# Optimization experiments

Measured on AMD Instinct MI355X. Metric: run time of the kernel, lower is better.

The kernel has to match this reference:

```python
import jax, jax.numpy as jnp
import numpy as np
from jax import lax

CH = 128
COND_CH = 80
N_LAYERS = 4
KSIZE = 3
KC = CH * CH * KSIZE * N_LAYERS  # 196608 kernel channels
BC = CH * N_LAYERS               # 512 bias channels


def _conv1d(x, w, b, padding, dilation=1):
    # x: [B, Cin, T], w: [Cout, Cin, K], b: [Cout]
    y = lax.conv_general_dilated(
        x, w, window_strides=(1,), padding=[(padding, padding)],
        rhs_dilation=(dilation,), dimension_numbers=("NCW", "OIW", "NCW"))
    return y + b[None, :, None]


def setup_inputs() -> dict:
    key = jax.random.key(0)
    ks = jax.random.split(key, 10)
    B, T_audio, T_mel = 8, 16384, 32
    scale = 0.02
    return {
        "x": jax.random.normal(ks[0], (B, CH, T_audio), jnp.float32),
        "cond": jax.random.normal(ks[1], (B, COND_CH, T_mel), jnp.float32),
        # predictor net params
        "w0": jax.random.normal(ks[2], (64, COND_CH, 5), jnp.float32) * scale,
        "b0": jnp.zeros((64,), jnp.float32),
        "w1": jax.random.normal(ks[3], (64, 64, 3), jnp.float32) * scale,
        "b1": jnp.zeros((64,), jnp.float32),
        "w2": jax.random.normal(ks[4], (KC + BC, 64, 1), jnp.float32) * scale,
        "b2": jnp.zeros((KC + BC,), jnp.float32),
        # snake activation param
        "alpha": jnp.ones((1, CH, 1), jnp.float32),
    }


def reference(x, cond, w0, b0, w1, b1, w2, b2, alpha):
    # --- kernel predictor ---
    h = jax.nn.gelu(_conv1d(cond, w0, b0, padding=2), approximate=False)
    h = jax.nn.gelu(_conv1d(h, w1, b1, padding=1), approximate=False)
    out = _conv1d(h, w2, b2, padding=0)          # [B, KC+BC, T_mel]
    kernels_flat = out[:, :KC]                    # [B, KC, T_mel]
    biases_flat = out[:, KC:]                     # [B, BC, T_mel]

    B = x.shape[0]
    k_per_layer = CH * CH * KSIZE

    def per_sample_conv(xi, ki, dilation, pad):
        # xi: [ch, T], ki: [ch, ch, ksize]
        y = lax.conv_general_dilated(
            xi[None], ki, window_strides=(1,), padding=[(pad, pad)],
            rhs_dilation=(dilation,), dimension_numbers=("NCW", "OIW", "NCW"))
        return y[0]

    for i in range(N_LAYERS):
        k_flat = kernels_flat[:, i * k_per_layer:(i + 1) * k_per_layer]
        b_flat = biases_flat[:, i * CH:(i + 1) * CH]
        dilation = 2 ** i
        pad = dilation * (KSIZE - 1) // 2
        k_mean = k_flat.mean(axis=-1).reshape(B, CH, CH, KSIZE)
        b_mean = b_flat.mean(axis=-1)             # [B, ch]
        y = jax.vmap(per_sample_conv, in_axes=(0, 0, None, None))(x, k_mean, dilation, pad)
        x = y + b_mean[:, :, None] + x            # conv(+bias) with residual

    # snake activation: x + 1/(alpha+eps) * sin(alpha*x)^2
    return x + 1.0 / (alpha + 1e-08) * jnp.sin(alpha * x) ** 2
```

## Files before the change

kernel.cpp:

```cpp
#include <hip/hip_runtime.h>
#include <math.h>

#define CHN 128
#define TT 16384
#define NBATCH 8
#define KCONST 196608
#define TILE_T 64
#define GUARD 8
#define CRANGE 96
#define ROWS 112
#define LROW 136

typedef __bf16 bf16x8 __attribute__((ext_vector_type(8)));
typedef float  f32x4  __attribute__((ext_vector_type(4)));
typedef unsigned short u16x8 __attribute__((ext_vector_type(8)));
typedef unsigned short u16x4 __attribute__((ext_vector_type(4)));

__device__ __forceinline__ unsigned short f2bf(float f) {
    union { float f; unsigned int u; } v; v.f = f;
    unsigned int u = v.u;
    u += 0x7fffu + ((u >> 16) & 1u);
    return (unsigned short)(u >> 16);
}
__device__ __forceinline__ float b2f(unsigned short h) {
    union { float f; unsigned int u; } v; v.u = ((unsigned int)h) << 16;
    return v.f;
}

__device__ __forceinline__ float gelu_exact(float x) {
    return 0.5f * x * (1.0f + erff(x * 0.70710678118654752f));
}

__global__ __launch_bounds__(256) void k_cond0(
    const float* __restrict__ cond, const float* __restrict__ w0,
    const float* __restrict__ b0, float* __restrict__ h0)
{
    __shared__ float cS[80 * 32];
    __shared__ float wS[8 * 80 * 5];
    __shared__ float bS[8];
    int b = blockIdx.x >> 3, g = blockIdx.x & 7;
    int tid = threadIdx.x;

    for (int idx = tid; idx < 80 * 32; idx += 256) cS[idx] = cond[b * 2560 + idx];
    for (int idx = tid; idx < 8 * 400; idx += 256) wS[idx] = w0[g * 3200 + idx];
    if (tid < 8) bS[tid] = b0[g * 8 + tid];
    __syncthreads();

    int oc = tid >> 5, t = tid & 31;
    float acc = bS[oc];
    const float* wr = wS + oc * 400;
    for (int ic = 0; ic < 80; ++ic) {
        const float* cr = cS + ic * 32;
        #pragma unroll
        for (int j = 0; j < 5; ++j) {
            int tv = t - 2 + j;
            if (tv >= 0 && tv < 32) acc += wr[ic * 5 + j] * cr[tv];
        }
    }
    h0[(b * 64 + g * 8 + oc) * 32 + t] = gelu_exact(acc);
}

__global__ __launch_bounds__(256) void k_cond1(
    const float* __restrict__ h0, const float* __restrict__ w1,
    const float* __restrict__ b1, float* __restrict__ hbar)
{
    __shared__ float hS[64 * 32];
    __shared__ float wS[8 * 64 * 3];
    __shared__ float bS[8];
    int b = blockIdx.x >> 3, g = blockIdx.x & 7;
    int tid = threadIdx.x;

    for (int idx = tid; idx < 64 * 32; idx += 256) hS[idx] = h0[b * 2048 + idx];
    for (int idx = tid; idx < 8 * 192; idx += 256) wS[idx] = w1[g * 1536 + idx];
    if (tid < 8) bS[tid] = b1[g * 8 + tid];
    __syncthreads();

    int oc = tid >> 5, t = tid & 31;
    float acc = bS[oc];
    const float* wr = wS + oc * 192;
    for (int ic = 0; ic < 64; ++ic) {
        const float* hr = hS + ic * 32;
        #pragma unroll
        for (int j = 0; j < 3; ++j) {
            int tv = t - 1 + j;
            if (tv >= 0 && tv < 32) acc += wr[ic * 3 + j] * hr[tv];
        }
    }
    float v = gelu_exact(acc);
    #pragma unroll
    for (int off = 1; off < 32; off <<= 1) v += __shfl_xor(v, off, 64);
    if (t == 0) hbar[b * 64 + g * 8 + oc] = v * (1.0f / 32.0f);
}

__global__ __launch_bounds__(256) void k_weights(
    const float* __restrict__ w2, const float* __restrict__ b2,
    const float* __restrict__ hbar,
    unsigned short* __restrict__ W, float* __restrict__ bmean)
{
    __shared__ float hS[8 * 64];
    __shared__ float buf[256 * 68];
    int tid = threadIdx.x;
    for (int idx = tid; idx < 512; idx += 256) hS[idx] = hbar[idx];

    const float4* src4 = (const float4*)(w2 + (long)blockIdx.x * 16384);
    #pragma unroll
    for (int it = 0; it < 16; ++it) {
        int f = it * 256 + tid;
        float4 v = src4[f];
        int row = f >> 4, col = f & 15;
        *(float4*)&buf[row * 68 + col * 4] = v;
    }
    __syncthreads();

    long p = (long)blockIdx.x * 256 + tid;
    const float* rowp = &buf[tid * 68];
    float acc[8];
    #pragma unroll
    for (int bb = 0; bb < 8; ++bb) acc[bb] = 0.f;
    #pragma unroll
    for (int q = 0; q < 16; ++q) {
        float4 wv = *(const float4*)&rowp[q * 4];
        #pragma unroll
        for (int bb = 0; bb < 8; ++bb) {
            const float* h = hS + bb * 64 + q * 4;
            acc[bb] += wv.x * h[0] + wv.y * h[1] + wv.z * h[2] + wv.w * h[3];
        }
    }
    float bias = b2[p];
    if (p < KCONST) {
        int i = (int)(p / 49152); int r = (int)(p % 49152);
        int o = r / 384; int m = r % 384; int c = m / 3; int tp = m % 3;
        #pragma unroll
        for (int bb = 0; bb < 8; ++bb)
            W[(long)((bb * 4 + i) * 128 + o) * 384 + tp * 128 + c] =
                f2bf(acc[bb] + bias);
    } else {
        int q = (int)(p - KCONST); int i = q >> 7, o = q & 127;
        #pragma unroll
        for (int bb = 0; bb < 8; ++bb)
            bmean[(bb * 4 + i) * 128 + o] = acc[bb] + bias;
    }
}

__global__ __launch_bounds__(256, 2) void k_fused(
    const float* __restrict__ src, float* __restrict__ dst,
    const unsigned short* __restrict__ W, const float* __restrict__ bmean,
    const float* __restrict__ alpha)
{
    __shared__ __align__(16) unsigned short xhi[ROWS * LROW];
    __shared__ __align__(16) unsigned short xlo[ROWS * LROW];

    int tid  = threadIdx.x;
    int lane = tid & 63;
    int wave = tid >> 6;
    int b    = blockIdx.x >> 8;
    int tile = blockIdx.x & 255;
    int T0   = tile * TILE_T;

    int nrow = lane & 15;
    int quad = lane >> 4;
    int o0   = wave * 32;

    const float* xb = src + (long)b * CHN * TT;

    {
        int cb = wave * 32;
        #pragma unroll 1
        for (int pass = 0; pass < 2; ++pass) {
            int tl = pass * 64 + lane;
            if (tl < ROWS) {
                int tg = T0 - 24 + tl;
                bool ok = (tg >= 0) && (tg < TT);
                #pragma unroll
                for (int kb = 0; kb < 4; ++kb) {
                    float v[8];
                    #pragma unroll
                    for (int k = 0; k < 8; ++k)
                        v[k] = ok ? xb[(long)(cb + kb * 8 + k) * TT + tg] : 0.f;
                    u16x8 h, l;
                    #pragma unroll
                    for (int k = 0; k < 8; ++k) {
                        h[k] = f2bf(v[k]);
                        l[k] = f2bf(v[k] - b2f(h[k]));
                    }
                    *(u16x8*)&xhi[tl * LROW + cb + kb * 8] = h;
                    *(u16x8*)&xlo[tl * LROW + cb + kb * 8] = l;
                }
            }
        }
    }

    float aval[2][4];
    #pragma unroll
    for (int mt = 0; mt < 2; ++mt)
        #pragma unroll
        for (int r = 0; r < 4; ++r)
            aval[mt][r] = alpha[o0 + mt * 16 + quad * 4 + r];

    __syncthreads();

    #pragma unroll 1
    for (int l = 0; l < 4; ++l) {
        const int d = 1 << l;
        const unsigned short* Wl = W + (long)((b * 4 + l) * 128) * 384;
        const float* bm = bmean + (b * 4 + l) * 128;

        bf16x8 af[2][12];
        #pragma unroll
        for (int mt = 0; mt < 2; ++mt) {
            const unsigned short* wr =
                Wl + (long)(o0 + mt * 16 + nrow) * 384 + quad * 8;
            #pragma unroll
            for (int ks = 0; ks < 12; ++ks)
                af[mt][ks] = *(const bf16x8*)(wr + ks * 32);
        }
        float bias[2][4];
        #pragma unroll
        for (int mt = 0; mt < 2; ++mt)
            #pragma unroll
            for (int r = 0; r < 4; ++r)
                bias[mt][r] = bm[o0 + mt * 16 + quad * 4 + r];

        f32x4 acc[2][6];
        #pragma unroll
        for (int mt = 0; mt < 2; ++mt)
            #pragma unroll
            for (int nt = 0; nt < 6; ++nt)
                acc[mt][nt] = (f32x4){0.f, 0.f, 0.f, 0.f};

        #pragma unroll
        for (int ks = 0; ks < 12; ++ks) {
            const int c0 = (ks & 3) * 32 + quad * 8;
            const int roff = GUARD + nrow + ((ks >> 2) - 1) * d;
            #pragma unroll
            for (int nt = 0; nt < 6; ++nt) {
                bf16x8 bf = *(const bf16x8*)&xhi[(roff + nt * 16) * LROW + c0];
                acc[0][nt] = __builtin_amdgcn_mfma_f32_16x16x32_bf16(
                    af[0][ks], bf, acc[0][nt], 0, 0, 0);
                acc[1][nt] = __builtin_amdgcn_mfma_f32_16x16x32_bf16(
                    af[1][ks], bf, acc[1][nt], 0, 0, 0);
            }
        }

        #pragma unroll
        for (int mt = 0; mt < 2; ++mt) {
            int obase = o0 + mt * 16 + quad * 4;
            #pragma unroll
            for (int nt = 0; nt < 6; ++nt) {
                int trow = GUARD + nt * 16 + nrow;
                u16x4 rh = *(const u16x4*)&xhi[trow * LROW + obase];
                u16x4 rl = *(const u16x4*)&xlo[trow * LROW + obase];
                #pragma unroll
                for (int r = 0; r < 4; ++r)
                    acc[mt][nt][r] += b2f(rh[r]) + b2f(rl[r]) + bias[mt][r];
            }
        }
        __syncthreads();

        if (l < 3) {
            #pragma unroll
            for (int mt = 0; mt < 2; ++mt) {
                int obase = o0 + mt * 16 + quad * 4;
                #pragma unroll
                for (int nt = 0; nt < 6; ++nt) {
                    int trow = GUARD + nt * 16 + nrow;
                    int tg = T0 - 16 + nt * 16 + nrow;
                    bool ok = ((unsigned)tg < (unsigned)TT);
                    u16x4 h, lo4;
                    #pragma unroll
                    for (int r = 0; r < 4; ++r) {
                        float v = ok ? acc[mt][nt][r] : 0.f;
                        h[r]   = f2bf(v);
                        lo4[r] = f2bf(v - b2f(h[r]));
                    }
                    *(u16x4*)&xhi[trow * LROW + obase] = h;
                    *(u16x4*)&xlo[trow * LROW + obase] = lo4;
                }
            }
            __syncthreads();
        } else {
            #pragma unroll
            for (int mt = 0; mt < 2; ++mt) {
                #pragma unroll
                for (int r = 0; r < 4; ++r) {
                    int o = o0 + mt * 16 + quad * 4 + r;
                    float av = aval[mt][r];
                    long rowoff = ((long)b * CHN + o) * TT + T0;
                    #pragma unroll
                    for (int nt = 1; nt < 5; ++nt) {
                        int t = (nt - 1) * 16 + nrow;
                        float xn = acc[mt][nt][r];
                        float s = sinf(av * xn);
                        dst[rowoff + t] = xn + (1.0f / (av + 1e-8f)) * s * s;
                    }
                }
            }
        }
    }
}

extern "C" void kernel_launch(void* const* d_in, const int* in_sizes, int n_in,
                              void* d_out, int out_size, void* d_ws, size_t ws_size,
                              hipStream_t stream) {
    const float* x     = (const float*)d_in[0];
    const float* cond  = (const float*)d_in[1];
    const float* w0    = (const float*)d_in[2];
    const float* b0    = (const float*)d_in[3];
    const float* w1    = (const float*)d_in[4];
    const float* b1    = (const float*)d_in[5];
    const float* w2    = (const float*)d_in[6];
    const float* b2    = (const float*)d_in[7];
    const float* alpha = (const float*)d_in[8];
    float* out = (float*)d_out;

    char* ws = (char*)d_ws;
    unsigned short* W = (unsigned short*)ws;
    float* bmean = (float*)(ws + 3145728);
    float* hbar  = (float*)(ws + 3162112);
    float* h0    = (float*)(ws + 3164160);

    k_cond0<<<64, 256, 0, stream>>>(cond, w0, b0, h0);
    k_cond1<<<64, 256, 0, stream>>>(h0, w1, b1, hbar);
    k_weights<<<772, 256, 0, stream>>>(w2, b2, hbar, W, bmean);
    k_fused<<<2048, 256, 0, stream>>>(x, out, W, bmean, alpha);
}
```

Measured before the change: 363.9 us.

## Carry residual in fp32 accumulators, drop lo LDS buffer, raise occupancy

Removes the second (low-bits) shared-memory activation buffer. The residual is now kept in fp32 accumulators that persist across layers, and layer 0 reads the input residual straight from global memory. This halves LDS use and stops preloading all weight fragments into registers, which allows launch_bounds of 4 blocks per CU. Weight fragments are loaded from global memory per k-step, and the final snake activation uses __sinf with a hoisted reciprocal, trading some accuracy for speed.

```diff
diff --git a/kernel.cpp b/kernel.cpp
--- a/kernel.cpp
+++ b/kernel.cpp
@@ -142,13 +142,12 @@
     }
 }
 
-__global__ __launch_bounds__(256, 2) void k_fused(
+__global__ __launch_bounds__(256, 4) void k_fused(
     const float* __restrict__ src, float* __restrict__ dst,
     const unsigned short* __restrict__ W, const float* __restrict__ bmean,
     const float* __restrict__ alpha)
 {
     __shared__ __align__(16) unsigned short xhi[ROWS * LROW];
-    __shared__ __align__(16) unsigned short xlo[ROWS * LROW];
 
     int tid  = threadIdx.x;
     int lane = tid & 63;
@@ -177,25 +176,21 @@
                     #pragma unroll
                     for (int k = 0; k < 8; ++k)
                         v[k] = ok ? xb[(long)(cb + kb * 8 + k) * TT + tg] : 0.f;
-                    u16x8 h, l;
-                    #pragma unroll
-                    for (int k = 0; k < 8; ++k) {
-                        h[k] = f2bf(v[k]);
-                        l[k] = f2bf(v[k] - b2f(h[k]));
-                    }
+                    u16x8 h;
+                    #pragma unroll
+                    for (int k = 0; k < 8; ++k) h[k] = f2bf(v[k]);
                     *(u16x8*)&xhi[tl * LROW + cb + kb * 8] = h;
-                    *(u16x8*)&xlo[tl * LROW + cb + kb * 8] = l;
-                }
-            }
-        }
-    }
-
-    float aval[2][4];
+                }
+            }
+        }
+    }
+
+    f32x4 acc[2][6];
     #pragma unroll
     for (int mt = 0; mt < 2; ++mt)
         #pragma unroll
-        for (int r = 0; r < 4; ++r)
-            aval[mt][r] = alpha[o0 + mt * 16 + quad * 4 + r];
+        for (int nt = 0; nt < 6; ++nt)
+            acc[mt][nt] = (f32x4){0.f, 0.f, 0.f, 0.f};
 
     __syncthreads();
 
@@ -205,54 +200,55 @@
         const unsigned short* Wl = W + (long)((b * 4 + l) * 128) * 384;
         const float* bm = bmean + (b * 4 + l) * 128;
 
-        bf16x8 af[2][12];
-        #pragma unroll
-        for (int mt = 0; mt < 2; ++mt) {
-            const unsigned short* wr =
-                Wl + (long)(o0 + mt * 16 + nrow) * 384 + quad * 8;
-            #pragma unroll
-            for (int ks = 0; ks < 12; ++ks)
-                af[mt][ks] = *(const bf16x8*)(wr + ks * 32);
-        }
-        float bias[2][4];
-        #pragma unroll
-        for (int mt = 0; mt < 2; ++mt)
-            #pragma unroll
-            for (int r = 0; r < 4; ++r)
-                bias[mt][r] = bm[o0 + mt * 16 + quad * 4 + r];
-
-        f32x4 acc[2][6];
-        #pragma unroll
-        for (int mt = 0; mt < 2; ++mt)
-            #pragma unroll
-            for (int nt = 0; nt < 6; ++nt)
-                acc[mt][nt] = (f32x4){0.f, 0.f, 0.f, 0.f};
-
         #pragma unroll
         for (int ks = 0; ks < 12; ++ks) {
             const int c0 = (ks & 3) * 32 + quad * 8;
             const int roff = GUARD + nrow + ((ks >> 2) - 1) * d;
+            const unsigned short* wr =
+                Wl + (long)(o0 + nrow) * 384 + ks * 32 + quad * 8;
+            bf16x8 a0 = *(const bf16x8*)(wr);
+            bf16x8 a1 = *(const bf16x8*)(wr + 16 * 384);
             #pragma unroll
             for (int nt = 0; nt < 6; ++nt) {
                 bf16x8 bf = *(const bf16x8*)&xhi[(roff + nt * 16) * LROW + c0];
                 acc[0][nt] = __builtin_amdgcn_mfma_f32_16x16x32_bf16(
-                    af[0][ks], bf, acc[0][nt], 0, 0, 0);
+                    a0, bf, acc[0][nt], 0, 0, 0);
                 acc[1][nt] = __builtin_amdgcn_mfma_f32_16x16x32_bf16(
-                    af[1][ks], bf, acc[1][nt], 0, 0, 0);
-            }
-        }
-
-        #pragma unroll
-        for (int mt = 0; mt < 2; ++mt) {
-            int obase = o0 + mt * 16 + quad * 4;
-            #pragma unroll
-            for (int nt = 0; nt < 6; ++nt) {
-                int trow = GUARD + nt * 16 + nrow;
-                u16x4 rh = *(const u16x4*)&xhi[trow * LROW + obase];
-                u16x4 rl = *(const u16x4*)&xlo[trow * LROW + obase];
-                #pragma unroll
-                for (int r = 0; r < 4; ++r)
-                    acc[mt][nt][r] += b2f(rh[r]) + b2f(rl[r]) + bias[mt][r];
+                    a1, bf, acc[1][nt], 0, 0, 0);
+            }
+        }
+
+        if (l == 0) {
+            #pragma unroll
+            for (int mt = 0; mt < 2; ++mt) {
+                int obase = o0 + mt * 16 + quad * 4;
+                float bias[4];
+                #pragma unroll
+                for (int r = 0; r < 4; ++r) bias[r] = bm[obase + r];
+                #pragma unroll
+                for (int nt = 0; nt < 6; ++nt) {
+                    int tg = T0 - 16 + nt * 16 + nrow;
+                    bool ok = ((unsigned)tg < (unsigned)TT);
+                    #pragma unroll
+                    for (int r = 0; r < 4; ++r) {
+                        float xf = ok ? xb[(long)(obase + r) * TT + tg] : 0.f;
+                        acc[mt][nt][r] += xf + bias[r];
+                    }
+                }
+            }
+        } else {
+            #pragma unroll
+            for (int mt = 0; mt < 2; ++mt) {
+                int obase = o0 + mt * 16 + quad * 4;
+                float bias[4];
+                #pragma unroll
+                for (int r = 0; r < 4; ++r) bias[r] = bm[obase + r];
+                #pragma unroll
+                for (int nt = 0; nt < 6; ++nt) {
+                    #pragma unroll
+                    for (int r = 0; r < 4; ++r)
+                        acc[mt][nt][r] += bias[r];
+                }
             }
         }
         __syncthreads();
@@ -266,15 +262,13 @@
                     int trow = GUARD + nt * 16 + nrow;
                     int tg = T0 - 16 + nt * 16 + nrow;
                     bool ok = ((unsigned)tg < (unsigned)TT);
-                    u16x4 h, lo4;
+                    u16x4 h;
                     #pragma unroll
                     for (int r = 0; r < 4; ++r) {
                         float v = ok ? acc[mt][nt][r] : 0.f;
-                        h[r]   = f2bf(v);
-                        lo4[r] = f2bf(v - b2f(h[r]));
+                        h[r] = f2bf(v);
                     }
                     *(u16x4*)&xhi[trow * LROW + obase] = h;
-                    *(u16x4*)&xlo[trow * LROW + obase] = lo4;
                 }
             }
             __syncthreads();
@@ -284,14 +278,15 @@
                 #pragma unroll
                 for (int r = 0; r < 4; ++r) {
                     int o = o0 + mt * 16 + quad * 4 + r;
-                    float av = aval[mt][r];
+                    float av = alpha[o];
+                    float rcp = 1.0f / (av + 1e-8f);
                     long rowoff = ((long)b * CHN + o) * TT + T0;
                     #pragma unroll
                     for (int nt = 1; nt < 5; ++nt) {
                         int t = (nt - 1) * 16 + nrow;
                         float xn = acc[mt][nt][r];
-                        float s = sinf(av * xn);
-                        dst[rowoff + t] = xn + (1.0f / (av + 1e-8f)) * s * s;
+                        float s = __sinf(av * xn);
+                        dst[rowoff + t] = xn + rcp * s * s;
                     }
                 }
             }
```

Measured after the change: 380.8 us. 1.05x slower.
